# Optimization experiments

Hardware: AMD Instinct MI355X
Metric: run time of the kernel (lower is better)

The kernel has to match this reference:

```python
import jax, jax.numpy as jnp
import numpy as np
import math

B, S, E = 2, 512, 1024
G, H, Q, D, V = 4, 8, 16, 2, 16  # groups, heads, query_len, duplicates, values_len
N = 512  # number of neurons (kv length)
EPS = 1e-5


def setup_inputs() -> dict:
    key = jax.random.key(0)
    ks = jax.random.split(key, 8)
    return {
        "embeddings": jax.random.normal(ks[0], (B, S, E), jnp.float32),
        "keys": jax.random.normal(ks[1], (B, G, N, Q * H), jnp.float32),
        "values": jax.random.normal(ks[2], (B, G, N, V * H), jnp.float32),
        "conn_sub": jax.random.normal(ks[3], (B, G, H, S * D, N), jnp.float32),
        "Wq": jax.random.normal(ks[4], (E, G * Q * H * D), jnp.float32) * 0.02,
        "bq": jnp.zeros((G * Q * H * D,), jnp.float32),
        "ln_g": jnp.ones((G * V * H * D,), jnp.float32),
        "ln_b": jnp.zeros((G * V * H * D,), jnp.float32),
        "Wre": jax.random.normal(ks[5], (G * V * H * D, E), jnp.float32) * 0.02,
        "bre": jnp.zeros((E,), jnp.float32),
    }


def reference(embeddings, keys, values, conn_sub, Wq, bq, ln_g, ln_b, Wre, bre):
    # queries: [B,S,E] @ [E,GQHD] -> raw reshape (matches torch .view on contiguous)
    q = embeddings @ Wq + bq                       # [B,S,G*Q*H*D]
    q = q.reshape(B, G, S * D, Q, H)               # same memory order as torch view
    q = jnp.transpose(q, (0, 1, 4, 2, 3))          # [B,G,H,S*D,Q]

    k = keys.reshape(B, G, N, Q, H)
    k = jnp.transpose(k, (0, 1, 4, 3, 2))          # [B,G,H,Q,N]
    v = values.reshape(B, G, N, V, H)
    v = jnp.transpose(v, (0, 1, 4, 2, 3))          # [B,G,H,N,V]

    scores = jnp.matmul(q, k) / math.sqrt(Q)       # [B,G,H,S*D,N]
    probs = jax.nn.softmax(scores - conn_sub, axis=-1)
    out = jnp.matmul(probs, v)                     # [B,G,H,S*D,V]

    out = out.reshape(B, G, H, D, S, V)
    out = jnp.transpose(out, (0, 4, 1, 2, 3, 5))   # [B,S,G,H,D,V]
    out = out.reshape(B, S, G * H * D * V)

    # LayerNorm over last dim (eps matches torch LayerNorm default 1e-5)
    mu = jnp.mean(out, axis=-1, keepdims=True)
    var = jnp.mean(jnp.square(out - mu), axis=-1, keepdims=True)
    ln = (out - mu) * jax.lax.rsqrt(var + EPS) * ln_g + ln_b

    return ln @ Wre + bre                          # [B,S,E]
```

## Files before the change

### kernel.cpp

```cpp
#include <hip/hip_runtime.h>


typedef __attribute__((ext_vector_type(4))) short bf16x4;
typedef __attribute__((ext_vector_type(8))) short short8;
typedef __attribute__((ext_vector_type(8))) unsigned short ushort8;
typedef __attribute__((ext_vector_type(8))) __bf16 bf16x8_t;
typedef __attribute__((ext_vector_type(4))) float f32x4;

static __device__ __forceinline__ unsigned short f2bf(float f) {
  union { float f; unsigned u; } v; v.f = f;
  unsigned r = v.u + 0x7fffu + ((v.u >> 16) & 1u);
  return (unsigned short)(r >> 16);
}

#if defined(__has_builtin)
#if __has_builtin(__builtin_amdgcn_mfma_f32_16x16x16bf16_1k)
#define HAVE_MFMA16 1
#endif
#if __has_builtin(__builtin_amdgcn_mfma_f32_16x16x32_bf16)
#define HAVE_MFMA32 1
#endif
#endif

static __device__ __forceinline__ f32x4 mfma16(bf16x4 a, bf16x4 b, f32x4 c) {
#ifdef HAVE_MFMA16
  return __builtin_amdgcn_mfma_f32_16x16x16bf16_1k(a, b, c, 0, 0, 0);
#else
  f32x4 d;
  asm volatile("v_mfma_f32_16x16x16_bf16 %0, %1, %2, %3\n\t"
               "s_nop 7\n\ts_nop 7"
               : "=&v"(d)
               : "v"(a), "v"(b), "v"(c));
  return d;
#endif
}

#ifdef HAVE_MFMA32
static __device__ __forceinline__ f32x4 mfma32(short8 a, short8 b, f32x4 c) {
  return __builtin_amdgcn_mfma_f32_16x16x32_bf16(
      __builtin_bit_cast(bf16x8_t, a), __builtin_bit_cast(bf16x8_t, b), c, 0, 0, 0);
}
#endif

__global__ __launch_bounds__(256) void prep_all(
    const float* __restrict__ Wq, const float* __restrict__ Wre,
    const float* __restrict__ keys, const float* __restrict__ values,
    const float* __restrict__ emb,
    unsigned short* __restrict__ WqT, unsigned short* __restrict__ WreT,
    unsigned short* __restrict__ KTb, unsigned short* __restrict__ VTb,
    unsigned short* __restrict__ embb) {
  __shared__ __align__(16) unsigned short t[64][72];
  const int blk = blockIdx.x;
  const int tid = threadIdx.x;

  if (blk < 512) {
    const float* W = (blk < 256) ? Wq : Wre;
    unsigned short* WT = (blk < 256) ? WqT : WreT;
    const int idx = blk & 255;
    const int bx = (idx & 15) * 64, by = (idx >> 4) * 64;
    const int r = tid >> 2;
    const int c0 = (tid & 3) * 16;
#pragma unroll
    for (int j = 0; j < 16; j += 4) {
      float4 v = *reinterpret_cast<const float4*>(&W[(long)(by + r) * 1024 + bx + c0 + j]);
      t[c0 + j + 0][r] = f2bf(v.x);
      t[c0 + j + 1][r] = f2bf(v.y);
      t[c0 + j + 2][r] = f2bf(v.z);
      t[c0 + j + 3][r] = f2bf(v.w);
    }
    __syncthreads();
#pragma unroll
    for (int j = 0; j < 16; j += 8) {
      *reinterpret_cast<ushort8*>(&WT[(long)(bx + r) * 1024 + by + c0 + j]) =
          *reinterpret_cast<const ushort8*>(&t[r][c0 + j]);
    }
  } else if (blk < 576) {
    const int kvIdx = blk - 512;
    const int bg = kvIdx >> 3, nb = kvIdx & 7;
    const long src_base = (long)bg * 512 * 128 + (long)nb * 64 * 128;
#pragma unroll
    for (int i = 0; i < 8; ++i) {
      int idx = tid + i * 256;
      int nl = idx >> 5, c4 = idx & 31;
      int n = nb * 64 + nl;
      float4 kv = *reinterpret_cast<const float4*>(&keys[src_base + nl * 128 + c4 * 4]);
      float4 vv = *reinterpret_cast<const float4*>(&values[src_base + nl * 128 + c4 * 4]);
      float kk[4] = {kv.x, kv.y, kv.z, kv.w};
      float vl[4] = {vv.x, vv.y, vv.z, vv.w};
#pragma unroll
      for (int cc = 0; cc < 4; ++cc) {
        int col = c4 * 4 + cc;
        int h = col & 7, qv = col >> 3;
        int bgh = bg * 8 + h;
        KTb[((long)bgh * 512 + n) * 16 + qv] = f2bf(kk[cc]);
        VTb[((long)bgh * 16 + qv) * 512 + n] = f2bf(vl[cc]);
      }
    }
  } else {
    const long i = ((long)(blk - 576) * 256 + tid) * 8;
    float4 a = *reinterpret_cast<const float4*>(&emb[i]);
    float4 b = *reinterpret_cast<const float4*>(&emb[i + 4]);
    ushort8 o;
    o[0] = f2bf(a.x); o[1] = f2bf(a.y); o[2] = f2bf(a.z); o[3] = f2bf(a.w);
    o[4] = f2bf(b.x); o[5] = f2bf(b.y); o[6] = f2bf(b.z); o[7] = f2bf(b.w);
    *reinterpret_cast<ushort8*>(&embb[i]) = o;
  }
}

template <int MODE>
__global__ __launch_bounds__(128) void gemm_bf16(
    const unsigned short* __restrict__ A, const unsigned short* __restrict__ BT,
    const float* __restrict__ bias, void* __restrict__ Cout) {
  __shared__ __align__(16) unsigned short As[2][32][72];
  __shared__ __align__(16) unsigned short Bs[2][32][72];
  const int tid = threadIdx.x;
  const int bid = blockIdx.x;
  const int tile = ((bid & 7) << 7) | (bid >> 3);
  const int brow = (tile >> 5) << 5, bcol = (tile & 31) << 5;
  const int lane = tid & 63, w = tid >> 6;
  const int fr = lane & 15, kg = lane >> 4;

  const int r0 = tid >> 3;
  const int r1 = r0 + 16;
  const int c0 = (tid & 7) * 8;

  const unsigned short* ap0 = A + (long)(brow + r0) * 1024 + c0;
  const unsigned short* ap1 = A + (long)(brow + r1) * 1024 + c0;
  const unsigned short* bp0 = BT + (long)(bcol + r0) * 1024 + c0;
  const unsigned short* bp1 = BT + (long)(bcol + r1) * 1024 + c0;

  f32x4 acc[2] = {{0.f, 0.f, 0.f, 0.f}, {0.f, 0.f, 0.f, 0.f}};

  ushort8 sa0 = *reinterpret_cast<const ushort8*>(ap0);
  ushort8 sa1 = *reinterpret_cast<const ushort8*>(ap1);
  ushort8 sb0 = *reinterpret_cast<const ushort8*>(bp0);
  ushort8 sb1 = *reinterpret_cast<const ushort8*>(bp1);
  int buf = 0;
  for (int kt = 0; kt < 1024; kt += 64) {
    *reinterpret_cast<ushort8*>(&As[buf][r0][c0]) = sa0;
    *reinterpret_cast<ushort8*>(&As[buf][r1][c0]) = sa1;
    *reinterpret_cast<ushort8*>(&Bs[buf][r0][c0]) = sb0;
    *reinterpret_cast<ushort8*>(&Bs[buf][r1][c0]) = sb1;
    __syncthreads();
    if (kt + 64 < 1024) {
      sa0 = *reinterpret_cast<const ushort8*>(ap0 + kt + 64);
      sa1 = *reinterpret_cast<const ushort8*>(ap1 + kt + 64);
      sb0 = *reinterpret_cast<const ushort8*>(bp0 + kt + 64);
      sb1 = *reinterpret_cast<const ushort8*>(bp1 + kt + 64);
    }
#ifdef HAVE_MFMA32
    short8 alo = *reinterpret_cast<const short8*>(&As[buf][(w << 4) + fr][kg * 8]);
    short8 ahi = *reinterpret_cast<const short8*>(&As[buf][(w << 4) + fr][32 + kg * 8]);
    short8 b0lo = *reinterpret_cast<const short8*>(&Bs[buf][fr][kg * 8]);
    short8 b0hi = *reinterpret_cast<const short8*>(&Bs[buf][fr][32 + kg * 8]);
    short8 b1lo = *reinterpret_cast<const short8*>(&Bs[buf][16 + fr][kg * 8]);
    short8 b1hi = *reinterpret_cast<const short8*>(&Bs[buf][16 + fr][32 + kg * 8]);
    acc[0] = mfma32(alo, b0lo, acc[0]);
    acc[1] = mfma32(alo, b1lo, acc[1]);
    acc[0] = mfma32(ahi, b0hi, acc[0]);
    acc[1] = mfma32(ahi, b1hi, acc[1]);
#else
#pragma unroll
    for (int kq = 0; kq < 4; ++kq) {
      bf16x4 a = *reinterpret_cast<const bf16x4*>(&As[buf][(w << 4) + fr][kq * 16 + kg * 4]);
      bf16x4 b0 = *reinterpret_cast<const bf16x4*>(&Bs[buf][fr][kq * 16 + kg * 4]);
      bf16x4 b1 = *reinterpret_cast<const bf16x4*>(&Bs[buf][16 + fr][kq * 16 + kg * 4]);
      acc[0] = mfma16(a, b0, acc[0]);
      acc[1] = mfma16(a, b1, acc[1]);
    }
#endif
    buf ^= 1;
  }

  const int mrow = brow + (w << 4) + kg * 4;
  if (MODE == 0) {
    float* C = (float*)Cout;
#pragma unroll
    for (int n = 0; n < 2; ++n) {
      const int colc = bcol + n * 16 + fr;
      const float bv = bias[colc];
#pragma unroll
      for (int j = 0; j < 4; ++j)
        C[(long)(mrow + j) * 1024 + colc] = acc[n][j] + bv;
    }
  } else {
    unsigned short* C = (unsigned short*)Cout;
#pragma unroll
    for (int n = 0; n < 2; ++n) {
      const int colc = bcol + n * 16 + fr;
      const float bv = bias[colc];
      const int h = colc & 7, qqi = (colc >> 3) & 15, chi = colc >> 7;
#pragma unroll
      for (int j = 0; j < 4; ++j) {
        int row = mrow + j;
        int b = row >> 9, s = row & 511, g = s >> 7;
        int sd = (s & 127) * 8 + chi;
        int bgh = b * 32 + g * 8 + h;
        C[((long)bgh * 1024 + sd) * 16 + qqi] = f2bf(acc[n][j] + bv);
      }
    }
  }
}

__global__ __launch_bounds__(256) void attn_mfma(
    const unsigned short* __restrict__ qTb, const unsigned short* __restrict__ KTb,
    const unsigned short* __restrict__ VTb, const float* __restrict__ conn,
    float* __restrict__ ln_in) {
  __shared__ float O_lds[4][16][17];

  const int tid = threadIdx.x;
  const int wid = tid >> 6, lane = tid & 63;
  const int c = lane & 15, hi = lane >> 4;
  const int rb = blockIdx.x;
  const int bgh = blockIdx.y;
  const int b = bgh >> 5, g = (bgh >> 3) & 3, h = bgh & 7;
  const int sd = rb * 64 + wid * 16 + c;

  bf16x4 qb = *reinterpret_cast<const bf16x4*>(&qTb[((long)bgh * 1024 + sd) * 16 + hi * 4]);

  const unsigned short* kp = KTb + (long)bgh * 8192 + hi * 4;
  const unsigned short* vp = VTb + (long)bgh * 8192 + (long)c * 512 + hi * 4;
  const float* cp = conn + ((long)bgh * 1024 + sd) * 512 + hi * 4;

  f32x4 acc = {0.f, 0.f, 0.f, 0.f};
  float m = -1e30f, lsum = 0.f;

  for (int nb = 0; nb < 512; nb += 64) {
    f32x4 sv[4];
    float cv[16];
    const f32x4 zero = {0.f, 0.f, 0.f, 0.f};
#pragma unroll
    for (int t = 0; t < 4; ++t) {
      const int n0 = nb + t * 16;
      bf16x4 ka = *reinterpret_cast<const bf16x4*>(kp + (long)(n0 + c) * 16);
      float4 cf = *reinterpret_cast<const float4*>(cp + n0);
      sv[t] = mfma16(ka, qb, zero);
      cv[t * 4 + 0] = cf.x;
      cv[t * 4 + 1] = cf.y;
      cv[t * 4 + 2] = cf.z;
      cv[t * 4 + 3] = cf.w;
    }
    float s[16];
#pragma unroll
    for (int t = 0; t < 4; ++t)
#pragma unroll
      for (int r = 0; r < 4; ++r) s[t * 4 + r] = sv[t][r] * 0.25f - cv[t * 4 + r];

    float cmax = s[0];
#pragma unroll
    for (int j = 1; j < 16; ++j) cmax = fmaxf(cmax, s[j]);
    cmax = fmaxf(cmax, __shfl_xor(cmax, 16, 64));
    cmax = fmaxf(cmax, __shfl_xor(cmax, 32, 64));
    const float mnew = fmaxf(m, cmax);
    const float fac = __expf(m - mnew);
    acc *= fac;
    lsum *= fac;
    float p[16];
    float csum = 0.f;
#pragma unroll
    for (int j = 0; j < 16; ++j) {
      p[j] = __expf(s[j] - mnew);
      csum += p[j];
    }
    lsum += csum;
    m = mnew;
#pragma unroll
    for (int t = 0; t < 4; ++t) {
      const int n0 = nb + t * 16;
      bf16x4 pb;
      pb[0] = (short)f2bf(p[t * 4 + 0]);
      pb[1] = (short)f2bf(p[t * 4 + 1]);
      pb[2] = (short)f2bf(p[t * 4 + 2]);
      pb[3] = (short)f2bf(p[t * 4 + 3]);
      bf16x4 va = *reinterpret_cast<const bf16x4*>(vp + n0);
      acc = mfma16(va, pb, acc);
    }
  }

  lsum += __shfl_xor(lsum, 16, 64);
  lsum += __shfl_xor(lsum, 32, 64);
  const float rinv = 1.0f / lsum;
#pragma unroll
  for (int r = 0; r < 4; ++r) O_lds[wid][c][hi * 4 + r] = acc[r] * rinv;
  __syncthreads();

  const int dd = (rb * 64) >> 9;
  const int chb = g * 256 + h * 32 + dd * 16;
#pragma unroll
  for (int pass = 0; pass < 4; ++pass) {
    int rr = pass * 16 + (tid >> 4);
    int v = tid & 15;
    int ssi = (rb * 64 + rr) & 511;
    ln_in[(long)(b * 512 + ssi) * 1024 + chb + v] = O_lds[rr >> 4][rr & 15][v];
  }
}

__global__ __launch_bounds__(256) void ln_kernel(
    const float* __restrict__ x, const float* __restrict__ gamma,
    const float* __restrict__ beta, unsigned short* __restrict__ out) {
  const int row = blockIdx.x;
  const int tid = threadIdx.x;
  float4 v = *reinterpret_cast<const float4*>(&x[(long)row * 1024 + tid * 4]);
  float s = v.x + v.y + v.z + v.w;
  float s2 = v.x * v.x + v.y * v.y + v.z * v.z + v.w * v.w;
#pragma unroll
  for (int w = 32; w >= 1; w >>= 1) {
    s += __shfl_xor(s, w, 64);
    s2 += __shfl_xor(s2, w, 64);
  }
  __shared__ float red[8];
  const int lane = tid & 63, wid = tid >> 6;
  if (lane == 0) {
    red[wid] = s;
    red[wid + 4] = s2;
  }
  __syncthreads();
  s = red[0] + red[1] + red[2] + red[3];
  s2 = red[4] + red[5] + red[6] + red[7];
  const float mu = s * (1.0f / 1024.0f);
  const float var = s2 * (1.0f / 1024.0f) - mu * mu;
  const float rstd = rsqrtf(var + 1e-5f);
  float4 g4 = *reinterpret_cast<const float4*>(&gamma[tid * 4]);
  float4 b4 = *reinterpret_cast<const float4*>(&beta[tid * 4]);
  unsigned short o[4];
  o[0] = f2bf((v.x - mu) * rstd * g4.x + b4.x);
  o[1] = f2bf((v.y - mu) * rstd * g4.y + b4.y);
  o[2] = f2bf((v.z - mu) * rstd * g4.z + b4.z);
  o[3] = f2bf((v.w - mu) * rstd * g4.w + b4.w);
  *reinterpret_cast<uint2*>(&out[(long)row * 1024 + tid * 4]) = *reinterpret_cast<uint2*>(o);
}

extern "C" void kernel_launch(void* const* d_in, const int* in_sizes, int n_in,
                              void* d_out, int out_size, void* d_ws,
                              size_t ws_size, hipStream_t stream) {
  const float* emb = (const float*)d_in[0];
  const float* keys = (const float*)d_in[1];
  const float* values = (const float*)d_in[2];
  const float* conn = (const float*)d_in[3];
  const float* Wq = (const float*)d_in[4];
  const float* bq = (const float*)d_in[5];
  const float* ln_g = (const float*)d_in[6];
  const float* ln_b = (const float*)d_in[7];
  const float* Wre = (const float*)d_in[8];
  const float* bre = (const float*)d_in[9];
  float* out = (float*)d_out;

  char* w = (char*)d_ws;
  float* ws_ln = (float*)w;
  unsigned short* ws_Ab = (unsigned short*)(w + 4 * 1024 * 1024);
  unsigned short* ws_WqT = (unsigned short*)(w + 6 * 1024 * 1024);
  unsigned short* ws_WreT = (unsigned short*)(w + 8 * 1024 * 1024);
  unsigned short* ws_qTb = (unsigned short*)(w + 10 * 1024 * 1024);
  unsigned short* ws_KTb = (unsigned short*)(w + 12 * 1024 * 1024);
  unsigned short* ws_VTb = (unsigned short*)(w + 13 * 1024 * 1024);

  prep_all<<<1088, 256, 0, stream>>>(Wq, Wre, keys, values, emb,
                                     ws_WqT, ws_WreT, ws_KTb, ws_VTb, ws_Ab);
  gemm_bf16<1><<<1024, 128, 0, stream>>>(ws_Ab, ws_WqT, bq, ws_qTb);
  attn_mfma<<<dim3(16, 64), 256, 0, stream>>>(ws_qTb, ws_KTb, ws_VTb, conn, ws_ln);
  ln_kernel<<<1024, 256, 0, stream>>>(ws_ln, ln_g, ln_b, ws_Ab);
  gemm_bf16<0><<<1024, 128, 0, stream>>>(ws_Ab, ws_WreT, bre, out);
}
```

Baseline: 75.92 us.

## Fuse query projection GEMM into attention kernel and prefetch conn tiles

Result: slower. 92.70 us (+22.1%).

```diff
diff --git a/kernel.cpp b/kernel.cpp
--- a/kernel.cpp
+++ b/kernel.cpp
@@ -45,17 +45,14 @@
 __global__ __launch_bounds__(256) void prep_all(
     const float* __restrict__ Wq, const float* __restrict__ Wre,
     const float* __restrict__ keys, const float* __restrict__ values,
-    const float* __restrict__ emb,
-    unsigned short* __restrict__ WqT, unsigned short* __restrict__ WreT,
-    unsigned short* __restrict__ KTb, unsigned short* __restrict__ VTb,
-    unsigned short* __restrict__ embb) {
+    unsigned short* __restrict__ WqP, unsigned short* __restrict__ WreT,
+    unsigned short* __restrict__ KTb, unsigned short* __restrict__ VTb) {
   __shared__ __align__(16) unsigned short t[64][72];
   const int blk = blockIdx.x;
   const int tid = threadIdx.x;
 
   if (blk < 512) {
     const float* W = (blk < 256) ? Wq : Wre;
-    unsigned short* WT = (blk < 256) ? WqT : WreT;
     const int idx = blk & 255;
     const int bx = (idx & 15) * 64, by = (idx >> 4) * 64;
     const int r = tid >> 2;
@@ -69,12 +66,23 @@
       t[c0 + j + 3][r] = f2bf(v.w);
     }
     __syncthreads();
+    const int cg = bx + r;
+    long dstbase;
+    unsigned short* dst;
+    if (blk < 256) {
+      const int h = cg & 7, qq = (cg >> 3) & 15, chi = cg >> 7;
+      dstbase = ((long)h * 128 + (chi * 16 + qq)) * 1024;
+      dst = WqP;
+    } else {
+      dstbase = (long)cg * 1024;
+      dst = WreT;
+    }
 #pragma unroll
     for (int j = 0; j < 16; j += 8) {
-      *reinterpret_cast<ushort8*>(&WT[(long)(bx + r) * 1024 + by + c0 + j]) =
+      *reinterpret_cast<ushort8*>(&dst[dstbase + by + c0 + j]) =
           *reinterpret_cast<const ushort8*>(&t[r][c0 + j]);
     }
-  } else if (blk < 576) {
+  } else {
     const int kvIdx = blk - 512;
     const int bg = kvIdx >> 3, nb = kvIdx & 7;
     const long src_base = (long)bg * 512 * 128 + (long)nb * 64 * 128;
@@ -96,21 +104,207 @@
         VTb[((long)bgh * 16 + qv) * 512 + n] = f2bf(vl[cc]);
       }
     }
-  } else {
-    const long i = ((long)(blk - 576) * 256 + tid) * 8;
-    float4 a = *reinterpret_cast<const float4*>(&emb[i]);
-    float4 b = *reinterpret_cast<const float4*>(&emb[i + 4]);
+  }
+}
+
+__global__ __launch_bounds__(256) void attn_fused(
+    const float* __restrict__ emb, const unsigned short* __restrict__ WqP,
+    const float* __restrict__ bq, const unsigned short* __restrict__ KTb,
+    const unsigned short* __restrict__ VTb, const float* __restrict__ conn,
+    float* __restrict__ ln_in) {
+  __shared__ __align__(16) unsigned short emb_lds[8 * 1032];
+  __shared__ __align__(16) unsigned short qlds[64][16];
+  __shared__ float O_lds[4][16][17];
+
+  const int tid = threadIdx.x;
+  const int wid = tid >> 6, lane = tid & 63;
+  const int c = lane & 15, hi = lane >> 4;
+  const int rb = blockIdx.x;
+  const int bgh = blockIdx.y;
+  const int b = bgh >> 5, g = (bgh >> 3) & 3, h = bgh & 7;
+
+  const long erow0 = (long)b * 512 + g * 128 + rb * 8;
+#pragma unroll
+  for (int i = 0; i < 4; ++i) {
+    int idx = tid + i * 256;
+    int row = idx >> 7, c8 = (idx & 127) * 8;
+    const float* p = emb + (erow0 + row) * 1024 + c8;
+    float4 a = *reinterpret_cast<const float4*>(p);
+    float4 bb = *reinterpret_cast<const float4*>(p + 4);
     ushort8 o;
     o[0] = f2bf(a.x); o[1] = f2bf(a.y); o[2] = f2bf(a.z); o[3] = f2bf(a.w);
-    o[4] = f2bf(b.x); o[5] = f2bf(b.y); o[6] = f2bf(b.z); o[7] = f2bf(b.w);
-    *reinterpret_cast<ushort8*>(&embb[i]) = o;
-  }
-}
-
-template <int MODE>
-__global__ __launch_bounds__(128) void gemm_bf16(
+    o[4] = f2bf(bb.x); o[5] = f2bf(bb.y); o[6] = f2bf(bb.z); o[7] = f2bf(bb.w);
+    *reinterpret_cast<ushort8*>(&emb_lds[row * 1032 + c8]) = o;
+  }
+  __syncthreads();
+
+  const int fr = c, kg = hi;
+  f32x4 qacc0 = {0.f, 0.f, 0.f, 0.f}, qacc1 = {0.f, 0.f, 0.f, 0.f};
+  const unsigned short* wqbase = WqP + (long)h * 131072;
+  const unsigned short* bpl0 = wqbase + (long)(wid * 32 + fr) * 1024 + kg * 8;
+  const unsigned short* bpl1 = bpl0 + 16 * 1024;
+  const int aoff = (fr & 7) * 1032 + kg * 8;
+#ifdef HAVE_MFMA32
+#pragma unroll 4
+  for (int kc = 0; kc < 32; ++kc) {
+    short8 af = *reinterpret_cast<const short8*>(&emb_lds[aoff + kc * 32]);
+    short8 b0 = *reinterpret_cast<const short8*>(bpl0 + kc * 32);
+    short8 b1 = *reinterpret_cast<const short8*>(bpl1 + kc * 32);
+    qacc0 = mfma32(af, b0, qacc0);
+    qacc1 = mfma32(af, b1, qacc1);
+  }
+#else
+  const int aoff4 = (fr & 7) * 1032 + kg * 4;
+  const unsigned short* bpl0a = wqbase + (long)(wid * 32 + fr) * 1024 + kg * 4;
+  const unsigned short* bpl1a = bpl0a + 16 * 1024;
+#pragma unroll 4
+  for (int kc = 0; kc < 64; ++kc) {
+    bf16x4 af = *reinterpret_cast<const bf16x4*>(&emb_lds[aoff4 + kc * 16]);
+    bf16x4 b0 = *reinterpret_cast<const bf16x4*>(bpl0a + kc * 16);
+    bf16x4 b1 = *reinterpret_cast<const bf16x4*>(bpl1a + kc * 16);
+    qacc0 = mfma16(af, b0, qacc0);
+    qacc1 = mfma16(af, b1, qacc1);
+  }
+#endif
+
+  if (hi < 2) {
+#pragma unroll
+    for (int t = 0; t < 2; ++t) {
+      const int chi = wid * 2 + t;
+      const float bqv = bq[chi * 128 + fr * 8 + h];
+      const f32x4 qa = t ? qacc1 : qacc0;
+#pragma unroll
+      for (int j = 0; j < 4; ++j) {
+        qlds[(hi * 4 + j) * 8 + chi][fr] = f2bf(qa[j] + bqv);
+      }
+    }
+  }
+  __syncthreads();
+
+  bf16x4 qb = *reinterpret_cast<const bf16x4*>(&qlds[wid * 16 + c][hi * 4]);
+
+  const unsigned short* kp = KTb + (long)bgh * 8192 + hi * 4;
+  const unsigned short* vp = VTb + (long)bgh * 8192 + (long)c * 512 + hi * 4;
+  const float* cp = conn + ((long)bgh * 1024 + rb * 64 + wid * 16 + c) * 512 + hi * 4;
+
+  f32x4 acc = {0.f, 0.f, 0.f, 0.f};
+  float m = -1e30f, lsum = 0.f;
+
+  float4 cvb[4];
+#pragma unroll
+  for (int t = 0; t < 4; ++t) cvb[t] = *reinterpret_cast<const float4*>(cp + t * 16);
+
+  for (int nb = 0; nb < 512; nb += 64) {
+    f32x4 sv[4];
+    const f32x4 zero = {0.f, 0.f, 0.f, 0.f};
+#pragma unroll
+    for (int t = 0; t < 4; ++t) {
+      bf16x4 ka = *reinterpret_cast<const bf16x4*>(kp + (long)(nb + t * 16 + c) * 16);
+      sv[t] = mfma16(ka, qb, zero);
+    }
+    float cv[16];
+#pragma unroll
+    for (int t = 0; t < 4; ++t) {
+      cv[t * 4 + 0] = cvb[t].x;
+      cv[t * 4 + 1] = cvb[t].y;
+      cv[t * 4 + 2] = cvb[t].z;
+      cv[t * 4 + 3] = cvb[t].w;
+    }
+    if (nb + 64 < 512) {
+#pragma unroll
+      for (int t = 0; t < 4; ++t)
+        cvb[t] = *reinterpret_cast<const float4*>(cp + nb + 64 + t * 16);
+    }
+    float s[16];
+#pragma unroll
+    for (int j = 0; j < 16; ++j) s[j] = sv[j >> 2][j & 3] * 0.25f - cv[j];
+
+    float cmax = s[0];
+#pragma unroll
+    for (int j = 1; j < 16; ++j) cmax = fmaxf(cmax, s[j]);
+    cmax = fmaxf(cmax, __shfl_xor(cmax, 16, 64));
+    cmax = fmaxf(cmax, __shfl_xor(cmax, 32, 64));
+    const float mnew = fmaxf(m, cmax);
+    const float fac = __expf(m - mnew);
+    acc *= fac;
+    lsum *= fac;
+    float p[16];
+    float csum = 0.f;
+#pragma unroll
+    for (int j = 0; j < 16; ++j) {
+      p[j] = __expf(s[j] - mnew);
+      csum += p[j];
+    }
+    lsum += csum;
+    m = mnew;
+#pragma unroll
+    for (int t = 0; t < 4; ++t) {
+      bf16x4 pb;
+      pb[0] = (short)f2bf(p[t * 4 + 0]);
+      pb[1] = (short)f2bf(p[t * 4 + 1]);
+      pb[2] = (short)f2bf(p[t * 4 + 2]);
+      pb[3] = (short)f2bf(p[t * 4 + 3]);
+      bf16x4 va = *reinterpret_cast<const bf16x4*>(vp + nb + t * 16);
+      acc = mfma16(va, pb, acc);
+    }
+  }
+
+  lsum += __shfl_xor(lsum, 16, 64);
+  lsum += __shfl_xor(lsum, 32, 64);
+  const float rinv = 1.0f / lsum;
+#pragma unroll
+  for (int r = 0; r < 4; ++r) O_lds[wid][c][hi * 4 + r] = acc[r] * rinv;
+  __syncthreads();
+
+  const int dd = (rb * 64) >> 9;
+  const int chb = g * 256 + h * 32 + dd * 16;
+#pragma unroll
+  for (int pass = 0; pass < 4; ++pass) {
+    int rr = pass * 16 + (tid >> 4);
+    int v = tid & 15;
+    int ssi = (rb * 64 + rr) & 511;
+    ln_in[(long)(b * 512 + ssi) * 1024 + chb + v] = O_lds[rr >> 4][rr & 15][v];
+  }
+}
+
+__global__ __launch_bounds__(256) void ln_kernel(
+    const float* __restrict__ x, const float* __restrict__ gamma,
+    const float* __restrict__ beta, unsigned short* __restrict__ out) {
+  const int row = blockIdx.x;
+  const int tid = threadIdx.x;
+  float4 v = *reinterpret_cast<const float4*>(&x[(long)row * 1024 + tid * 4]);
+  float s = v.x + v.y + v.z + v.w;
+  float s2 = v.x * v.x + v.y * v.y + v.z * v.z + v.w * v.w;
+#pragma unroll
+  for (int w = 32; w >= 1; w >>= 1) {
+    s += __shfl_xor(s, w, 64);
+    s2 += __shfl_xor(s2, w, 64);
+  }
+  __shared__ float red[8];
+  const int lane = tid & 63, wid = tid >> 6;
+  if (lane == 0) {
+    red[wid] = s;
+    red[wid + 4] = s2;
+  }
+  __syncthreads();
+  s = red[0] + red[1] + red[2] + red[3];
+  s2 = red[4] + red[5] + red[6] + red[7];
+  const float mu = s * (1.0f / 1024.0f);
+  const float var = s2 * (1.0f / 1024.0f) - mu * mu;
+  const float rstd = rsqrtf(var + 1e-5f);
+  float4 g4 = *reinterpret_cast<const float4*>(&gamma[tid * 4]);
+  float4 b4 = *reinterpret_cast<const float4*>(&beta[tid * 4]);
+  unsigned short o[4];
+  o[0] = f2bf((v.x - mu) * rstd * g4.x + b4.x);
+  o[1] = f2bf((v.y - mu) * rstd * g4.y + b4.y);
+  o[2] = f2bf((v.z - mu) * rstd * g4.z + b4.z);
+  o[3] = f2bf((v.w - mu) * rstd * g4.w + b4.w);
+  *reinterpret_cast<uint2*>(&out[(long)row * 1024 + tid * 4]) = *reinterpret_cast<uint2*>(o);
+}
+
+__global__ __launch_bounds__(128) void gemm_out(
     const unsigned short* __restrict__ A, const unsigned short* __restrict__ BT,
-    const float* __restrict__ bias, void* __restrict__ Cout) {
+    const float* __restrict__ bias, float* __restrict__ C) {
   __shared__ __align__(16) unsigned short As[2][32][72];
   __shared__ __align__(16) unsigned short Bs[2][32][72];
   const int tid = threadIdx.x;
@@ -173,161 +367,14 @@
   }
 
   const int mrow = brow + (w << 4) + kg * 4;
-  if (MODE == 0) {
-    float* C = (float*)Cout;
-#pragma unroll
-    for (int n = 0; n < 2; ++n) {
-      const int colc = bcol + n * 16 + fr;
-      const float bv = bias[colc];
-#pragma unroll
-      for (int j = 0; j < 4; ++j)
-        C[(long)(mrow + j) * 1024 + colc] = acc[n][j] + bv;
-    }
-  } else {
-    unsigned short* C = (unsigned short*)Cout;
-#pragma unroll
-    for (int n = 0; n < 2; ++n) {
-      const int colc = bcol + n * 16 + fr;
-      const float bv = bias[colc];
-      const int h = colc & 7, qqi = (colc >> 3) & 15, chi = colc >> 7;
-#pragma unroll
-      for (int j = 0; j < 4; ++j) {
-        int row = mrow + j;
-        int b = row >> 9, s = row & 511, g = s >> 7;
-        int sd = (s & 127) * 8 + chi;
-        int bgh = b * 32 + g * 8 + h;
-        C[((long)bgh * 1024 + sd) * 16 + qqi] = f2bf(acc[n][j] + bv);
-      }
-    }
-  }
-}
-
-__global__ __launch_bounds__(256) void attn_mfma(
-    const unsigned short* __restrict__ qTb, const unsigned short* __restrict__ KTb,
-    const unsigned short* __restrict__ VTb, const float* __restrict__ conn,
-    float* __restrict__ ln_in) {
-  __shared__ float O_lds[4][16][17];
-
-  const int tid = threadIdx.x;
-  const int wid = tid >> 6, lane = tid & 63;
-  const int c = lane & 15, hi = lane >> 4;
-  const int rb = blockIdx.x;
-  const int bgh = blockIdx.y;
-  const int b = bgh >> 5, g = (bgh >> 3) & 3, h = bgh & 7;
-  const int sd = rb * 64 + wid * 16 + c;
-
-  bf16x4 qb = *reinterpret_cast<const bf16x4*>(&qTb[((long)bgh * 1024 + sd) * 16 + hi * 4]);
-
-  const unsigned short* kp = KTb + (long)bgh * 8192 + hi * 4;
-  const unsigned short* vp = VTb + (long)bgh * 8192 + (long)c * 512 + hi * 4;
-  const float* cp = conn + ((long)bgh * 1024 + sd) * 512 + hi * 4;
-
-  f32x4 acc = {0.f, 0.f, 0.f, 0.f};
-  float m = -1e30f, lsum = 0.f;
-
-  for (int nb = 0; nb < 512; nb += 64) {
-    f32x4 sv[4];
-    float cv[16];
-    const f32x4 zero = {0.f, 0.f, 0.f, 0.f};
-#pragma unroll
-    for (int t = 0; t < 4; ++t) {
-      const int n0 = nb + t * 16;
-      bf16x4 ka = *reinterpret_cast<const bf16x4*>(kp + (long)(n0 + c) * 16);
-      float4 cf = *reinterpret_cast<const float4*>(cp + n0);
-      sv[t] = mfma16(ka, qb, zero);
-      cv[t * 4 + 0] = cf.x;
-      cv[t * 4 + 1] = cf.y;
-      cv[t * 4 + 2] = cf.z;
-      cv[t * 4 + 3] = cf.w;
-    }
-    float s[16];
-#pragma unroll
-    for (int t = 0; t < 4; ++t)
-#pragma unroll
-      for (int r = 0; r < 4; ++r) s[t * 4 + r] = sv[t][r] * 0.25f - cv[t * 4 + r];
-
-    float cmax = s[0];
-#pragma unroll
-    for (int j = 1; j < 16; ++j) cmax = fmaxf(cmax, s[j]);
-    cmax = fmaxf(cmax, __shfl_xor(cmax, 16, 64));
-    cmax = fmaxf(cmax, __shfl_xor(cmax, 32, 64));
-    const float mnew = fmaxf(m, cmax);
-    const float fac = __expf(m - mnew);
-    acc *= fac;
-    lsum *= fac;
-    float p[16];
-    float csum = 0.f;
-#pragma unroll
-    for (int j = 0; j < 16; ++j) {
-      p[j] = __expf(s[j] - mnew);
-      csum += p[j];
-    }
-    lsum += csum;
-    m = mnew;
-#pragma unroll
-    for (int t = 0; t < 4; ++t) {
-      const int n0 = nb + t * 16;
-      bf16x4 pb;
-      pb[0] = (short)f2bf(p[t * 4 + 0]);
-      pb[1] = (short)f2bf(p[t * 4 + 1]);
-      pb[2] = (short)f2bf(p[t * 4 + 2]);
-      pb[3] = (short)f2bf(p[t * 4 + 3]);
-      bf16x4 va = *reinterpret_cast<const bf16x4*>(vp + n0);
-      acc = mfma16(va, pb, acc);
-    }
-  }
-
-  lsum += __shfl_xor(lsum, 16, 64);
-  lsum += __shfl_xor(lsum, 32, 64);
-  const float rinv = 1.0f / lsum;
-#pragma unroll
-  for (int r = 0; r < 4; ++r) O_lds[wid][c][hi * 4 + r] = acc[r] * rinv;
-  __syncthreads();
-
-  const int dd = (rb * 64) >> 9;
-  const int chb = g * 256 + h * 32 + dd * 16;
-#pragma unroll
-  for (int pass = 0; pass < 4; ++pass) {
-    int rr = pass * 16 + (tid >> 4);
-    int v = tid & 15;
-    int ssi = (rb * 64 + rr) & 511;
-    ln_in[(long)(b * 512 + ssi) * 1024 + chb + v] = O_lds[rr >> 4][rr & 15][v];
-  }
-}
-
-__global__ __launch_bounds__(256) void ln_kernel(
-    const float* __restrict__ x, const float* __restrict__ gamma,
-    const float* __restrict__ beta, unsigned short* __restrict__ out) {
-  const int row = blockIdx.x;
-  const int tid = threadIdx.x;
-  float4 v = *reinterpret_cast<const float4*>(&x[(long)row * 1024 + tid * 4]);
-  float s = v.x + v.y + v.z + v.w;
-  float s2 = v.x * v.x + v.y * v.y + v.z * v.z + v.w * v.w;
-#pragma unroll
-  for (int w = 32; w >= 1; w >>= 1) {
-    s += __shfl_xor(s, w, 64);
-    s2 += __shfl_xor(s2, w, 64);
-  }
-  __shared__ float red[8];
-  const int lane = tid & 63, wid = tid >> 6;
-  if (lane == 0) {
-    red[wid] = s;
-    red[wid + 4] = s2;
-  }
-  __syncthreads();
-  s = red[0] + red[1] + red[2] + red[3];
-  s2 = red[4] + red[5] + red[6] + red[7];
-  const float mu = s * (1.0f / 1024.0f);
-  const float var = s2 * (1.0f / 1024.0f) - mu * mu;
-  const float rstd = rsqrtf(var + 1e-5f);
-  float4 g4 = *reinterpret_cast<const float4*>(&gamma[tid * 4]);
-  float4 b4 = *reinterpret_cast<const float4*>(&beta[tid * 4]);
-  unsigned short o[4];
-  o[0] = f2bf((v.x - mu) * rstd * g4.x + b4.x);
-  o[1] = f2bf((v.y - mu) * rstd * g4.y + b4.y);
-  o[2] = f2bf((v.z - mu) * rstd * g4.z + b4.z);
-  o[3] = f2bf((v.w - mu) * rstd * g4.w + b4.w);
-  *reinterpret_cast<uint2*>(&out[(long)row * 1024 + tid * 4]) = *reinterpret_cast<uint2*>(o);
+#pragma unroll
+  for (int n = 0; n < 2; ++n) {
+    const int colc = bcol + n * 16 + fr;
+    const float bv = bias[colc];
+#pragma unroll
+    for (int j = 0; j < 4; ++j)
+      C[(long)(mrow + j) * 1024 + colc] = acc[n][j] + bv;
+  }
 }
 
 extern "C" void kernel_launch(void* const* d_in, const int* in_sizes, int n_in,
@@ -348,16 +395,15 @@
   char* w = (char*)d_ws;
   float* ws_ln = (float*)w;
   unsigned short* ws_Ab = (unsigned short*)(w + 4 * 1024 * 1024);
-  unsigned short* ws_WqT = (unsigned short*)(w + 6 * 1024 * 1024);
+  unsigned short* ws_WqP = (unsigned short*)(w + 6 * 1024 * 1024);
   unsigned short* ws_WreT = (unsigned short*)(w + 8 * 1024 * 1024);
-  unsigned short* ws_qTb = (unsigned short*)(w + 10 * 1024 * 1024);
-  unsigned short* ws_KTb = (unsigned short*)(w + 12 * 1024 * 1024);
-  unsigned short* ws_VTb = (unsigned short*)(w + 13 * 1024 * 1024);
-
-  prep_all<<<1088, 256, 0, stream>>>(Wq, Wre, keys, values, emb,
-                                     ws_WqT, ws_WreT, ws_KTb, ws_VTb, ws_Ab);
-  gemm_bf16<1><<<1024, 128, 0, stream>>>(ws_Ab, ws_WqT, bq, ws_qTb);
-  attn_mfma<<<dim3(16, 64), 256, 0, stream>>>(ws_qTb, ws_KTb, ws_VTb, conn, ws_ln);
+  unsigned short* ws_KTb = (unsigned short*)(w + 10 * 1024 * 1024);
+  unsigned short* ws_VTb = (unsigned short*)(w + 11 * 1024 * 1024);
+
+  prep_all<<<576, 256, 0, stream>>>(Wq, Wre, keys, values,
+                                    ws_WqP, ws_WreT, ws_KTb, ws_VTb);
+  attn_fused<<<dim3(16, 64), 256, 0, stream>>>(emb, ws_WqP, bq, ws_KTb, ws_VTb,
+                                               conn, ws_ln);
   ln_kernel<<<1024, 256, 0, stream>>>(ws_ln, ln_g, ln_b, ws_Ab);
-  gemm_bf16<0><<<1024, 128, 0, stream>>>(ws_Ab, ws_WreT, bre, out);
-}
+  gemm_out<<<1024, 128, 0, stream>>>(ws_Ab, ws_WreT, bre, out);
+}
```
